# Kernel tuning notes

Measured on AMD Instinct MI355X. Metric: run time of the kernel, lower is better.

Reference implementation:

```python
import jax, jax.numpy as jnp
import numpy as np

B = 32768
STATE_DIM = 64
ACTION_DIM = 16
HIDDEN = 512
ENSEMBLE = 7
TOP_K = 5
IN_DIM = STATE_DIM + ACTION_DIM          # 80
OUT_DIM = 2 * (STATE_DIM + 1)            # 130 (mu | log_std)


def setup_inputs() -> dict:
    key = jax.random.key(0)
    ks = jax.random.split(key, 12)
    state = jax.random.normal(ks[0], (B, STATE_DIM), dtype=jnp.float32)
    action = jax.random.normal(ks[1], (B, ACTION_DIM), dtype=jnp.float32)
    eps = jax.random.normal(ks[2], (B, STATE_DIM + 1), dtype=jnp.float32)
    # per-sample random expert among the selected subset [0, TOP_K)
    idx = jax.random.randint(ks[3], (B,), 0, TOP_K).astype(jnp.int64)
    # stacked expert params (kaiming-ish scale = 1/sqrt(fan_in))
    W1 = jax.random.normal(ks[4], (ENSEMBLE, IN_DIM, HIDDEN), dtype=jnp.float32) / np.sqrt(IN_DIM)
    b1 = jnp.zeros((ENSEMBLE, HIDDEN), dtype=jnp.float32)
    W2 = jax.random.normal(ks[5], (ENSEMBLE, HIDDEN, HIDDEN), dtype=jnp.float32) / np.sqrt(HIDDEN)
    b2 = jnp.zeros((ENSEMBLE, HIDDEN), dtype=jnp.float32)
    W3 = jax.random.normal(ks[6], (ENSEMBLE, HIDDEN, OUT_DIM), dtype=jnp.float32) / np.sqrt(HIDDEN)
    b3 = jnp.zeros((ENSEMBLE, OUT_DIM), dtype=jnp.float32)
    return {"state": state, "action": action, "eps": eps,
            "W1": W1, "b1": b1, "W2": W2, "b2": b2, "W3": W3, "b3": b3,
            "idx": idx}


def reference(state, action, eps, W1, b1, W2, b2, W3, b3, idx):
    # DynamicsEnsemble.predict: per-sample random expert, Gaussian sample.
    x = jnp.concatenate([state, action], axis=-1)            # [B, IN_DIM]
    # run all experts densely, then gather the routed expert per sample
    h = jax.nn.relu(jnp.einsum('bi,eih->beh', x, W1) + b1)   # [B, E, H]
    h = jax.nn.relu(jnp.einsum('beh,ehk->bek', h, W2) + b2)  # [B, E, H]
    o = jnp.einsum('bek,eko->beo', h, W3) + b3               # [B, E, OUT]
    out = jnp.take_along_axis(o, idx[:, None, None].astype(jnp.int32), axis=1)[:, 0]  # [B, OUT]
    d = state.shape[-1] + 1
    mu = out[:, :d]
    log_std = jnp.clip(out[:, d:], -20.0, 2.0)
    y = mu + jnp.exp(log_std) * eps                          # sampled [delta_state, reward]
    next_state = state + y[:, : state.shape[-1]]
    reward = y[:, state.shape[-1]:]                          # [B, 1]
    return next_state, reward
```

## Files before the change

### kernel.cpp

```cpp
#include <hip/hip_runtime.h>
#include <math.h>

#define B_ROWS     32768
#define STATE_DIM  64
#define ACTION_DIM 16
#define HIDDEN     512
#define ENSEMBLE   7
#define TOP_K      5
#define IN_DIM     80
#define OUT_DIM    130
#define D_OUT      65

#define BM         64
#define MTHREADS   1024
#define NTILES     (B_ROWS / BM + TOP_K)

#define L1_K8 12
#define L2_K8 64
#define L3_K8 64
#define L3_N  144

#define N_W1 (TOP_K * L1_K8 * HIDDEN * 8)
#define N_W2 (TOP_K * L2_K8 * HIDDEN * 8)
#define N_W3 (TOP_K * L3_K8 * L3_N * 8)

#define OFF_CNT    0
#define OFF_BUCKET 256
#define OFF_W1     (OFF_BUCKET + ENSEMBLE * B_ROWS * 4)
#define OFF_W2     (OFF_W1 + N_W1 * 2)
#define OFF_W3     (OFF_W2 + N_W2 * 2)
#define WS_NEEDED  ((size_t)(OFF_W3 + N_W3 * 2))

#define BUCKET_BLOCKS ((B_ROWS + 255) / 256)
#define PACK_G        (TOP_K * (L1_K8*HIDDEN + L2_K8*HIDDEN + L3_K8*L3_N))
#define PACK_BLOCKS   ((PACK_G + 255) / 256)

typedef __attribute__((ext_vector_type(8))) _Float16 half8;
typedef __attribute__((ext_vector_type(4))) float f32x4;

__global__ void prep_kernel(const int* __restrict__ idx,
                            int* __restrict__ cnt,
                            int* __restrict__ bucket,
                            const float* __restrict__ W1, const float* __restrict__ W2,
                            const float* __restrict__ W3,
                            _Float16* __restrict__ w1, _Float16* __restrict__ w2,
                            _Float16* __restrict__ w3) {
    if (blockIdx.x < BUCKET_BLOCKS) {
        int b = blockIdx.x * 256 + threadIdx.x;
        int lane = threadIdx.x & 63;
        int e = -1;
        if (b < B_ROWS) e = min(max(idx[b], 0), TOP_K - 1);
        #pragma unroll
        for (int ev = 0; ev < TOP_K; ++ev) {
            unsigned long long m = __ballot(e == ev);
            if (m == 0ull) continue;
            int leader = __ffsll((unsigned long long)m) - 1;
            int base = 0;
            if (lane == leader) base = atomicAdd(&cnt[ev], __popcll(m));
            base = __shfl(base, leader);
            if (e == ev) {
                int rank = __popcll(m & ((1ull << lane) - 1ull));
                bucket[ev * B_ROWS + base + rank] = b;
            }
        }
        return;
    }
    const int G1 = L1_K8 * HIDDEN;
    const int G2 = L2_K8 * HIDDEN;
    const int G3 = L3_K8 * L3_N;
    const int GPE = G1 + G2 + G3;
    int g = (blockIdx.x - BUCKET_BLOCKS) * 256 + threadIdx.x;
    if (g >= TOP_K * GPE) return;
    int e = g / GPE, r = g % GPE;

    const float* src; _Float16* dd;
    size_t dst; int k8, n, Kreal, Nreal, srcN;
    if (r < G1) {
        k8 = r / HIDDEN; n = r % HIDDEN;
        src = W1 + (size_t)e * IN_DIM * HIDDEN; Kreal = IN_DIM; Nreal = HIDDEN; srcN = HIDDEN;
        dd = w1; dst = (((size_t)e * L1_K8 + k8) * HIDDEN + n) * 8;
    } else if (r < G1 + G2) {
        int rr = r - G1; k8 = rr / HIDDEN; n = rr % HIDDEN;
        src = W2 + (size_t)e * HIDDEN * HIDDEN; Kreal = HIDDEN; Nreal = HIDDEN; srcN = HIDDEN;
        dd = w2; dst = (((size_t)e * L2_K8 + k8) * HIDDEN + n) * 8;
    } else {
        int rr = r - G1 - G2; k8 = rr / L3_N; n = rr % L3_N;
        src = W3 + (size_t)e * HIDDEN * OUT_DIM; Kreal = HIDDEN; Nreal = OUT_DIM; srcN = OUT_DIM;
        dd = w3; dst = (((size_t)e * L3_K8 + k8) * L3_N + n) * 8;
    }
    half8 hv;
    #pragma unroll
    for (int j = 0; j < 8; ++j) {
        int k = k8 * 8 + j;
        float v = (k < Kreal && n < Nreal) ? src[(size_t)k * srcN + n] : 0.f;
        hv[j] = (_Float16)v;
    }
    *(half8*)(dd + dst) = hv;
}

template<int ASTR, bool SWZ, int KSTEPS>
__device__ __forceinline__ void gemm_compute(
    const char* A,
    const _Float16* __restrict__ B, int Bn, const float* __restrict__ bias,
    f32x4 (&acc)[2][4], int lane, int row0, int col0)
{
    const int lc = lane & 15, kg = lane >> 4;
    #pragma unroll
    for (int ctl = 0; ctl < 4; ++ctl) {
        float b = bias[col0 + ctl * 16 + lc];
        acc[0][ctl] = (f32x4){b, b, b, b};
        acc[1][ctl] = acc[0][ctl];
    }
    const size_t bstep = (size_t)4 * Bn * 8;
    const _Float16* bp = B + ((size_t)kg * Bn + col0 + lc) * 8;

    #pragma unroll
    for (int ks = 0; ks < KSTEPS; ++ks) {
        half8 bc[4];
        #pragma unroll
        for (int ctl = 0; ctl < 4; ++ctl)
            bc[ctl] = *(const half8*)(bp + (size_t)ks * bstep + ctl * 128);
        half8 ah[2];
        #pragma unroll
        for (int rt = 0; rt < 2; ++rt) {
            int row = row0 + rt * 16 + lc;
            int lin = row * ASTR + ks * 64 + kg * 16;
            if (SWZ) lin ^= (row & 7) << 4;
            ah[rt] = *(const half8*)(A + lin);
        }
        #pragma unroll
        for (int rt = 0; rt < 2; ++rt)
        #pragma unroll
        for (int ctl = 0; ctl < 4; ++ctl)
            acc[rt][ctl] = __builtin_amdgcn_mfma_f32_16x16x32_f16(ah[rt], bc[ctl], acc[rt][ctl], 0, 0, 0);
    }
}

__device__ __forceinline__ void store_h(char* O, f32x4 (&acc)[2][4], int lane, int row0, int col0) {
    const int lc = lane & 15, kg = lane >> 4;
    #pragma unroll
    for (int rt = 0; rt < 2; ++rt)
    #pragma unroll
    for (int ctl = 0; ctl < 4; ++ctl)
    #pragma unroll
    for (int q = 0; q < 4; ++q) {
        int row = row0 + rt * 16 + kg * 4 + q;
        int col = col0 + ctl * 16 + lc;
        float v = fmaxf(acc[rt][ctl][q], 0.f);
        int lin = (row * 1024 + col * 2) ^ ((row & 7) << 4);
        *(_Float16*)(O + lin) = (_Float16)v;
    }
}

__device__ __forceinline__ int xcd_swz(int orig) {
    const int nx = 8, q = NTILES / nx, r = NTILES % nx;
    int xcd = orig % nx, pos = orig / nx;
    int base = (xcd < r) ? xcd * (q + 1) : r * (q + 1) + (xcd - r) * q;
    return base + pos;
}

__launch_bounds__(MTHREADS)
__global__ void mlp_mfma_kernel(const float* __restrict__ state,
                                const float* __restrict__ action,
                                const float* __restrict__ eps,
                                const float* __restrict__ b1,
                                const float* __restrict__ b2,
                                const float* __restrict__ b3,
                                const _Float16* __restrict__ w1,
                                const _Float16* __restrict__ w2,
                                const _Float16* __restrict__ w3,
                                const int* __restrict__ cnt, const int* __restrict__ bucket,
                                float* __restrict__ out) {
    __shared__ char smem[79872];
    char* xs = smem;
    char* hs = smem + 14336;
    float* os = (float*)(smem + 14336);

    const int j = xcd_swz(blockIdx.x);
    int e = TOP_K, base = 0;
    {
        int acct = 0;
        #pragma unroll
        for (int ev = 0; ev < TOP_K; ++ev) {
            int tiles = (cnt[ev] + BM - 1) / BM;
            if (e == TOP_K && j < acct + tiles) { e = ev; base = acct; }
            acct += tiles;
        }
    }
    if (e >= TOP_K) return;
    const int n    = cnt[e];
    const int tile = j - base;
    const int m0   = tile * BM;
    if (m0 >= n) return;
    const int nrows = min(BM, n - m0);
    const int t = threadIdx.x;
    const int lane = t & 63;
    const int wv = t >> 6;
    const int row0 = (wv >> 3) * 32;
    const int col0 = (wv & 7) * 64;
    const int* brow = bucket + (size_t)e * B_ROWS;

    for (int i = t; i < BM * 112; i += MTHREADS) {
        int r = i / 112, c = i % 112;
        int rb = brow[min(m0 + r, n - 1)];
        float v = 0.f;
        if (c < STATE_DIM)      v = state[(size_t)rb * STATE_DIM + c];
        else if (c < IN_DIM)    v = action[(size_t)rb * ACTION_DIM + (c - STATE_DIM)];
        *(_Float16*)(xs + r * 224 + c * 2) = (_Float16)v;
    }
    __syncthreads();

    f32x4 acc[2][4];

    gemm_compute<224, false, 3>(xs,
        w1 + (size_t)e * L1_K8 * HIDDEN * 8,
        HIDDEN, b1 + (size_t)e * HIDDEN, acc, lane, row0, col0);
    store_h(hs, acc, lane, row0, col0);
    __syncthreads();

    gemm_compute<1024, true, 16>(hs,
        w2 + (size_t)e * L2_K8 * HIDDEN * 8,
        HIDDEN, b2 + (size_t)e * HIDDEN, acc, lane, row0, col0);
    __syncthreads();
    store_h(hs, acc, lane, row0, col0);
    __syncthreads();

    {
        const _Float16* Bw = w3 + (size_t)e * L3_K8 * L3_N * 8;
        const float* b3e = b3 + (size_t)e * OUT_DIM;
        const int lc = lane & 15, kg = lane >> 4;
        const int rt  = wv & 3;
        const int ct0 = wv >> 2;
        const bool third = (wv < 4);
        f32x4 o0 = {0.f,0.f,0.f,0.f}, o1 = o0, o2 = o0;
        const size_t bstep = (size_t)4 * L3_N * 8;
        const _Float16* bp0 = Bw + ((size_t)kg * L3_N + ct0 * 16 + lc) * 8;
        const _Float16* bp1 = Bw + ((size_t)kg * L3_N + (ct0 + 4) * 16 + lc) * 8;
        const _Float16* bp2 = Bw + ((size_t)kg * L3_N + 8 * 16 + lc) * 8;

        #pragma unroll
        for (int ks = 0; ks < 16; ++ks) {
            int row = rt * 16 + lc;
            int lin = (row * 1024 + ks * 64 + kg * 16) ^ ((row & 7) << 4);
            half8 ah = *(const half8*)(hs + lin);
            half8 v0 = *(const half8*)(bp0 + (size_t)ks * bstep);
            half8 v1 = *(const half8*)(bp1 + (size_t)ks * bstep);
            o0 = __builtin_amdgcn_mfma_f32_16x16x32_f16(ah, v0, o0, 0, 0, 0);
            o1 = __builtin_amdgcn_mfma_f32_16x16x32_f16(ah, v1, o1, 0, 0, 0);
            if (third) {
                half8 v2 = *(const half8*)(bp2 + (size_t)ks * bstep);
                o2 = __builtin_amdgcn_mfma_f32_16x16x32_f16(ah, v2, o2, 0, 0, 0);
            }
        }
        __syncthreads();
        {
            int c0 = ct0 * 16 + lc;
            int c1 = (ct0 + 4) * 16 + lc;
            #pragma unroll
            for (int q = 0; q < 4; ++q) {
                int row = rt * 16 + kg * 4 + q;
                os[row * 132 + c0] = o0[q] + b3e[c0];
                if (c1 < OUT_DIM) os[row * 132 + c1] = o1[q] + b3e[c1];
            }
            if (third) {
                int c2 = 128 + lc;
                if (c2 < OUT_DIM) {
                    #pragma unroll
                    for (int q = 0; q < 4; ++q) {
                        int row = rt * 16 + kg * 4 + q;
                        os[row * 132 + c2] = o2[q] + b3e[c2];
                    }
                }
            }
        }
    }
    __syncthreads();

    for (int i = t; i < BM * D_OUT; i += MTHREADS) {
        int r = i / D_OUT, c = i % D_OUT;
        if (r >= nrows) continue;
        int rb = brow[m0 + r];
        float mu = os[r * 132 + c];
        float ls = fminf(fmaxf(os[r * 132 + c + D_OUT], -20.f), 2.f);
        float y  = fmaf(expf(ls), eps[(size_t)rb * D_OUT + c], mu);
        if (c < STATE_DIM) {
            out[(size_t)rb * STATE_DIM + c] = state[(size_t)rb * STATE_DIM + c] + y;
        } else {
            out[(size_t)B_ROWS * STATE_DIM + rb] = y;
        }
    }
}

#define FB_BM      16
#define FB_THREADS 256
#define FB_TILES   ((B_ROWS + FB_BM - 1) / FB_BM)

__launch_bounds__(FB_THREADS, 2)
__global__ void mlp_fp32_kernel(const float* __restrict__ state,
                                const float* __restrict__ action,
                                const float* __restrict__ eps,
                                const float* __restrict__ W1, const float* __restrict__ b1,
                                const float* __restrict__ W2, const float* __restrict__ b2,
                                const float* __restrict__ W3, const float* __restrict__ b3,
                                const int* __restrict__ cnt, const int* __restrict__ bucket,
                                float* __restrict__ out) {
    __shared__ float xs[FB_BM][IN_DIM];
    __shared__ float h1[FB_BM][HIDDEN];
    __shared__ float h2[FB_BM][HIDDEN];
    __shared__ float os[FB_BM][OUT_DIM];
    __shared__ int   rows[FB_BM];

    const int e    = blockIdx.x / FB_TILES;
    const int tile = blockIdx.x % FB_TILES;
    const int n    = cnt[e];
    const int m0   = tile * FB_BM;
    if (m0 >= n) return;
    const int nrows = min(FB_BM, n - m0);
    const int t = threadIdx.x;

    if (t < FB_BM) rows[t] = (t < nrows) ? bucket[e * B_ROWS + m0 + t] : bucket[e * B_ROWS + m0];
    __syncthreads();

    for (int i = t; i < FB_BM * IN_DIM; i += FB_THREADS) {
        int r = i / IN_DIM, c = i % IN_DIM;
        int rb = rows[r];
        xs[r][c] = (c < STATE_DIM) ? state[(size_t)rb * STATE_DIM + c]
                                   : action[(size_t)rb * ACTION_DIM + (c - STATE_DIM)];
    }
    __syncthreads();

    const int c0 = 2 * t;
    {
        const float* We = W1 + (size_t)e * IN_DIM * HIDDEN;
        float acc0[FB_BM], acc1[FB_BM];
        const float bias0 = b1[(size_t)e * HIDDEN + c0];
        const float bias1 = b1[(size_t)e * HIDDEN + c0 + 1];
        #pragma unroll
        for (int r = 0; r < FB_BM; ++r) { acc0[r] = bias0; acc1[r] = bias1; }
        for (int k = 0; k < IN_DIM; k += 4) {
            float2 w0 = *(const float2*)&We[(size_t)(k + 0) * HIDDEN + c0];
            float2 w1v = *(const float2*)&We[(size_t)(k + 1) * HIDDEN + c0];
            float2 w2v = *(const float2*)&We[(size_t)(k + 2) * HIDDEN + c0];
            float2 w3v = *(const float2*)&We[(size_t)(k + 3) * HIDDEN + c0];
            #pragma unroll
            for (int r = 0; r < FB_BM; ++r) {
                float4 x = *(const float4*)&xs[r][k];
                acc0[r] = fmaf(x.x, w0.x, acc0[r]); acc1[r] = fmaf(x.x, w0.y, acc1[r]);
                acc0[r] = fmaf(x.y, w1v.x, acc0[r]); acc1[r] = fmaf(x.y, w1v.y, acc1[r]);
                acc0[r] = fmaf(x.z, w2v.x, acc0[r]); acc1[r] = fmaf(x.z, w2v.y, acc1[r]);
                acc0[r] = fmaf(x.w, w3v.x, acc0[r]); acc1[r] = fmaf(x.w, w3v.y, acc1[r]);
            }
        }
        #pragma unroll
        for (int r = 0; r < FB_BM; ++r)
            *(float2*)&h1[r][c0] = make_float2(fmaxf(acc0[r], 0.f), fmaxf(acc1[r], 0.f));
    }
    __syncthreads();
    {
        const float* We = W2 + (size_t)e * HIDDEN * HIDDEN;
        float acc0[FB_BM], acc1[FB_BM];
        const float bias0 = b2[(size_t)e * HIDDEN + c0];
        const float bias1 = b2[(size_t)e * HIDDEN + c0 + 1];
        #pragma unroll
        for (int r = 0; r < FB_BM; ++r) { acc0[r] = bias0; acc1[r] = bias1; }
        for (int k = 0; k < HIDDEN; k += 4) {
            float2 w0 = *(const float2*)&We[(size_t)(k + 0) * HIDDEN + c0];
            float2 w1v = *(const float2*)&We[(size_t)(k + 1) * HIDDEN + c0];
            float2 w2v = *(const float2*)&We[(size_t)(k + 2) * HIDDEN + c0];
            float2 w3v = *(const float2*)&We[(size_t)(k + 3) * HIDDEN + c0];
            #pragma unroll
            for (int r = 0; r < FB_BM; ++r) {
                float4 x = *(const float4*)&h1[r][k];
                acc0[r] = fmaf(x.x, w0.x, acc0[r]); acc1[r] = fmaf(x.x, w0.y, acc1[r]);
                acc0[r] = fmaf(x.y, w1v.x, acc0[r]); acc1[r] = fmaf(x.y, w1v.y, acc1[r]);
                acc0[r] = fmaf(x.z, w2v.x, acc0[r]); acc1[r] = fmaf(x.z, w2v.y, acc1[r]);
                acc0[r] = fmaf(x.w, w3v.x, acc0[r]); acc1[r] = fmaf(x.w, w3v.y, acc1[r]);
            }
        }
        #pragma unroll
        for (int r = 0; r < FB_BM; ++r)
            *(float2*)&h2[r][c0] = make_float2(fmaxf(acc0[r], 0.f), fmaxf(acc1[r], 0.f));
    }
    __syncthreads();
    {
        const float* We = W3 + (size_t)e * HIDDEN * OUT_DIM;
        for (int i = t; i < FB_BM * OUT_DIM; i += FB_THREADS) {
            int r = i / OUT_DIM, c = i % OUT_DIM;
            float acc = b3[(size_t)e * OUT_DIM + c];
            for (int k = 0; k < HIDDEN; k += 4) {
                float4 h = *(const float4*)&h2[r][k];
                acc = fmaf(h.x, We[(size_t)(k + 0) * OUT_DIM + c], acc);
                acc = fmaf(h.y, We[(size_t)(k + 1) * OUT_DIM + c], acc);
                acc = fmaf(h.z, We[(size_t)(k + 2) * OUT_DIM + c], acc);
                acc = fmaf(h.w, We[(size_t)(k + 3) * OUT_DIM + c], acc);
            }
            os[r][c] = acc;
        }
    }
    __syncthreads();
    for (int i = t; i < FB_BM * D_OUT; i += FB_THREADS) {
        int r = i / D_OUT, c = i % D_OUT;
        if (r >= nrows) continue;
        int rb = rows[r];
        float mu = os[r][c];
        float ls = fminf(fmaxf(os[r][c + D_OUT], -20.f), 2.f);
        float y  = fmaf(expf(ls), eps[(size_t)rb * D_OUT + c], mu);
        if (c < STATE_DIM) out[(size_t)rb * STATE_DIM + c] = state[(size_t)rb * STATE_DIM + c] + y;
        else               out[(size_t)B_ROWS * STATE_DIM + rb] = y;
    }
}

extern "C" void kernel_launch(void* const* d_in, const int* in_sizes, int n_in,
                              void* d_out, int out_size, void* d_ws, size_t ws_size,
                              hipStream_t stream) {
    const float* state  = (const float*)d_in[0];
    const float* action = (const float*)d_in[1];
    const float* eps    = (const float*)d_in[2];
    const float* W1     = (const float*)d_in[3];
    const float* b1     = (const float*)d_in[4];
    const float* W2     = (const float*)d_in[5];
    const float* b2     = (const float*)d_in[6];
    const float* W3     = (const float*)d_in[7];
    const float* b3     = (const float*)d_in[8];
    const int*   idx    = (const int*)d_in[9];
    float* out = (float*)d_out;

    int* cnt    = (int*)((char*)d_ws + OFF_CNT);
    int* bucket = (int*)((char*)d_ws + OFF_BUCKET);

    hipMemsetAsync(cnt, 0, ENSEMBLE * sizeof(int), stream);

    if (ws_size >= WS_NEEDED) {
        _Float16* w1 = (_Float16*)((char*)d_ws + OFF_W1);
        _Float16* w2 = (_Float16*)((char*)d_ws + OFF_W2);
        _Float16* w3 = (_Float16*)((char*)d_ws + OFF_W3);

        prep_kernel<<<BUCKET_BLOCKS + PACK_BLOCKS, 256, 0, stream>>>(
            idx, cnt, bucket, W1, W2, W3, w1, w2, w3);

        mlp_mfma_kernel<<<NTILES, MTHREADS, 0, stream>>>(
            state, action, eps, b1, b2, b3, w1, w2, w3, cnt, bucket, out);
    } else {
        prep_kernel<<<BUCKET_BLOCKS, 256, 0, stream>>>(
            idx, cnt, bucket, W1, W2, W3, (_Float16*)0, (_Float16*)0, (_Float16*)0);
        mlp_fp32_kernel<<<TOP_K * FB_TILES, FB_THREADS, 0, stream>>>(
            state, action, eps, W1, b1, W2, b2, W3, b3, cnt, bucket, out);
    }
}
```

Measured before the change: 136.9 us.

## Halve block threads and give each wave a full 64-row by 64-column tile

Drops the block from 1024 to 512 threads (8 waves). Each wave now computes all 64 rows for its 64-column slice, using a 4x4 grid of MFMA accumulators instead of 2x4. This halves how often B weights are fetched per row and reuses each B fragment across four row tiles. The layer-3 split is rebalanced so each wave handles four or five column tiles. In exchange, per-thread register use roughly doubles, which can limit occupancy even with launch bounds asking for 4 blocks per CU, and there are fewer waves to hide latency.

Result: slower. 155.2 us (+13.3%).

```diff
diff --git a/kernel.cpp b/kernel.cpp
--- a/kernel.cpp
+++ b/kernel.cpp
@@ -12,7 +12,7 @@
 #define D_OUT      65
 
 #define BM         64
-#define MTHREADS   1024
+#define MTHREADS   512
 #define NTILES     (B_ROWS / BM + TOP_K)
 
 #define L1_K8 12
@@ -102,14 +102,14 @@
 __device__ __forceinline__ void gemm_compute(
     const char* A,
     const _Float16* __restrict__ B, int Bn, const float* __restrict__ bias,
-    f32x4 (&acc)[2][4], int lane, int row0, int col0)
+    f32x4 (&acc)[4][4], int lane, int col0)
 {
     const int lc = lane & 15, kg = lane >> 4;
     #pragma unroll
     for (int ctl = 0; ctl < 4; ++ctl) {
         float b = bias[col0 + ctl * 16 + lc];
-        acc[0][ctl] = (f32x4){b, b, b, b};
-        acc[1][ctl] = acc[0][ctl];
+        #pragma unroll
+        for (int rt = 0; rt < 4; ++rt) acc[rt][ctl] = (f32x4){b, b, b, b};
     }
     const size_t bstep = (size_t)4 * Bn * 8;
     const _Float16* bp = B + ((size_t)kg * Bn + col0 + lc) * 8;
@@ -120,31 +120,31 @@
         #pragma unroll
         for (int ctl = 0; ctl < 4; ++ctl)
             bc[ctl] = *(const half8*)(bp + (size_t)ks * bstep + ctl * 128);
-        half8 ah[2];
-        #pragma unroll
-        for (int rt = 0; rt < 2; ++rt) {
-            int row = row0 + rt * 16 + lc;
+        half8 ah[4];
+        #pragma unroll
+        for (int rt = 0; rt < 4; ++rt) {
+            int row = rt * 16 + lc;
             int lin = row * ASTR + ks * 64 + kg * 16;
             if (SWZ) lin ^= (row & 7) << 4;
             ah[rt] = *(const half8*)(A + lin);
         }
         #pragma unroll
-        for (int rt = 0; rt < 2; ++rt)
+        for (int rt = 0; rt < 4; ++rt)
         #pragma unroll
         for (int ctl = 0; ctl < 4; ++ctl)
             acc[rt][ctl] = __builtin_amdgcn_mfma_f32_16x16x32_f16(ah[rt], bc[ctl], acc[rt][ctl], 0, 0, 0);
     }
 }
 
-__device__ __forceinline__ void store_h(char* O, f32x4 (&acc)[2][4], int lane, int row0, int col0) {
+__device__ __forceinline__ void store_h(char* O, f32x4 (&acc)[4][4], int lane, int col0) {
     const int lc = lane & 15, kg = lane >> 4;
     #pragma unroll
-    for (int rt = 0; rt < 2; ++rt)
+    for (int rt = 0; rt < 4; ++rt)
     #pragma unroll
     for (int ctl = 0; ctl < 4; ++ctl)
     #pragma unroll
     for (int q = 0; q < 4; ++q) {
-        int row = row0 + rt * 16 + kg * 4 + q;
+        int row = rt * 16 + kg * 4 + q;
         int col = col0 + ctl * 16 + lc;
         float v = fmaxf(acc[rt][ctl][q], 0.f);
         int lin = (row * 1024 + col * 2) ^ ((row & 7) << 4);
@@ -159,7 +159,7 @@
     return base + pos;
 }
 
-__launch_bounds__(MTHREADS)
+__launch_bounds__(MTHREADS, 4)
 __global__ void mlp_mfma_kernel(const float* __restrict__ state,
                                 const float* __restrict__ action,
                                 const float* __restrict__ eps,
@@ -196,8 +196,7 @@
     const int t = threadIdx.x;
     const int lane = t & 63;
     const int wv = t >> 6;
-    const int row0 = (wv >> 3) * 32;
-    const int col0 = (wv & 7) * 64;
+    const int col0 = wv * 64;
     const int* brow = bucket + (size_t)e * B_ROWS;
 
     for (int i = t; i < BM * 112; i += MTHREADS) {
@@ -210,19 +209,19 @@
     }
     __syncthreads();
 
-    f32x4 acc[2][4];
+    f32x4 acc[4][4];
 
     gemm_compute<224, false, 3>(xs,
         w1 + (size_t)e * L1_K8 * HIDDEN * 8,
-        HIDDEN, b1 + (size_t)e * HIDDEN, acc, lane, row0, col0);
-    store_h(hs, acc, lane, row0, col0);
+        HIDDEN, b1 + (size_t)e * HIDDEN, acc, lane, col0);
+    store_h(hs, acc, lane, col0);
     __syncthreads();
 
     gemm_compute<1024, true, 16>(hs,
         w2 + (size_t)e * L2_K8 * HIDDEN * 8,
-        HIDDEN, b2 + (size_t)e * HIDDEN, acc, lane, row0, col0);
-    __syncthreads();
-    store_h(hs, acc, lane, row0, col0);
+        HIDDEN, b2 + (size_t)e * HIDDEN, acc, lane, col0);
+    __syncthreads();
+    store_h(hs, acc, lane, col0);
     __syncthreads();
 
     {
@@ -231,12 +230,14 @@
         const int lc = lane & 15, kg = lane >> 4;
         const int rt  = wv & 3;
         const int ct0 = wv >> 2;
-        const bool third = (wv < 4);
-        f32x4 o0 = {0.f,0.f,0.f,0.f}, o1 = o0, o2 = o0;
+        const bool fifth = (wv < 4);
+        f32x4 o0 = {0.f,0.f,0.f,0.f}, o1 = o0, o2 = o0, o3 = o0, o4 = o0;
         const size_t bstep = (size_t)4 * L3_N * 8;
-        const _Float16* bp0 = Bw + ((size_t)kg * L3_N + ct0 * 16 + lc) * 8;
-        const _Float16* bp1 = Bw + ((size_t)kg * L3_N + (ct0 + 4) * 16 + lc) * 8;
-        const _Float16* bp2 = Bw + ((size_t)kg * L3_N + 8 * 16 + lc) * 8;
+        const _Float16* bp0 = Bw + ((size_t)kg * L3_N + (ct0 + 0) * 16 + lc) * 8;
+        const _Float16* bp1 = Bw + ((size_t)kg * L3_N + (ct0 + 2) * 16 + lc) * 8;
+        const _Float16* bp2 = Bw + ((size_t)kg * L3_N + (ct0 + 4) * 16 + lc) * 8;
+        const _Float16* bp3 = Bw + ((size_t)kg * L3_N + (ct0 + 6) * 16 + lc) * 8;
+        const _Float16* bp4 = Bw + ((size_t)kg * L3_N + 8 * 16 + lc) * 8;
 
         #pragma unroll
         for (int ks = 0; ks < 16; ++ks) {
@@ -245,30 +246,38 @@
             half8 ah = *(const half8*)(hs + lin);
             half8 v0 = *(const half8*)(bp0 + (size_t)ks * bstep);
             half8 v1 = *(const half8*)(bp1 + (size_t)ks * bstep);
+            half8 v2 = *(const half8*)(bp2 + (size_t)ks * bstep);
+            half8 v3 = *(const half8*)(bp3 + (size_t)ks * bstep);
             o0 = __builtin_amdgcn_mfma_f32_16x16x32_f16(ah, v0, o0, 0, 0, 0);
             o1 = __builtin_amdgcn_mfma_f32_16x16x32_f16(ah, v1, o1, 0, 0, 0);
-            if (third) {
-                half8 v2 = *(const half8*)(bp2 + (size_t)ks * bstep);
-                o2 = __builtin_amdgcn_mfma_f32_16x16x32_f16(ah, v2, o2, 0, 0, 0);
+            o2 = __builtin_amdgcn_mfma_f32_16x16x32_f16(ah, v2, o2, 0, 0, 0);
+            o3 = __builtin_amdgcn_mfma_f32_16x16x32_f16(ah, v3, o3, 0, 0, 0);
+            if (fifth) {
+                half8 v4 = *(const half8*)(bp4 + (size_t)ks * bstep);
+                o4 = __builtin_amdgcn_mfma_f32_16x16x32_f16(ah, v4, o4, 0, 0, 0);
             }
         }
         __syncthreads();
         {
-            int c0 = ct0 * 16 + lc;
-            int c1 = (ct0 + 4) * 16 + lc;
+            int c0 = (ct0 + 0) * 16 + lc;
+            int c1 = (ct0 + 2) * 16 + lc;
+            int c2 = (ct0 + 4) * 16 + lc;
+            int c3 = (ct0 + 6) * 16 + lc;
             #pragma unroll
             for (int q = 0; q < 4; ++q) {
                 int row = rt * 16 + kg * 4 + q;
                 os[row * 132 + c0] = o0[q] + b3e[c0];
-                if (c1 < OUT_DIM) os[row * 132 + c1] = o1[q] + b3e[c1];
-            }
-            if (third) {
-                int c2 = 128 + lc;
-                if (c2 < OUT_DIM) {
+                os[row * 132 + c1] = o1[q] + b3e[c1];
+                os[row * 132 + c2] = o2[q] + b3e[c2];
+                os[row * 132 + c3] = o3[q] + b3e[c3];
+            }
+            if (fifth) {
+                int c4 = 128 + lc;
+                if (c4 < OUT_DIM) {
                     #pragma unroll
                     for (int q = 0; q < 4; ++q) {
                         int row = rt * 16 + kg * 4 + q;
-                        os[row * 132 + c2] = o2[q] + b3e[c2];
+                        os[row * 132 + c4] = o4[q] + b3e[c4];
                     }
                 }
             }
```

## Stage weight tiles into LDS with async global_load_lds double buffering

Applied to the files above, without the earlier changes.

Raises the row tile to 112 rows with 512 threads and one block per CU. Weights are repacked in prep into contiguous 16KB k-slices, which are streamed into two LDS buffers with global_load_lds while MFMAs run on the previous slice. Each wave now computes 7 row-tiles by 4 column-tiles, so every B fragment is reused across more rows and direct global weight reads from each wave are removed. The cost is much more LDS (144KB), a __syncthreads per k-slice, higher register pressure from 28 accumulators, and fewer waves per CU.

Measured after the change: 210.0 us. 1.53x slower.

```diff
diff --git a/kernel.cpp b/kernel.cpp
--- a/kernel.cpp
+++ b/kernel.cpp
@@ -11,8 +11,8 @@
 #define OUT_DIM    130
 #define D_OUT      65
 
-#define BM         64
-#define MTHREADS   1024
+#define BM         112
+#define MTHREADS   512
 #define NTILES     (B_ROWS / BM + TOP_K)
 
 #define L1_K8 12
@@ -37,6 +37,14 @@
 
 typedef __attribute__((ext_vector_type(8))) _Float16 half8;
 typedef __attribute__((ext_vector_type(4))) float f32x4;
+
+__device__ __forceinline__ void stage_tile(const char* g, char* l, int t, int bytes) {
+    for (int off = t * 16; off < bytes; off += MTHREADS * 16) {
+        __builtin_amdgcn_global_load_lds(
+            (const __attribute__((address_space(1))) void*)(g + off),
+            (__attribute__((address_space(3))) void*)(l + off), 16, 0, 0);
+    }
+}
 
 __global__ void prep_kernel(const int* __restrict__ idx,
                             int* __restrict__ cnt,
@@ -78,11 +86,15 @@
     if (r < G1) {
         k8 = r / HIDDEN; n = r % HIDDEN;
         src = W1 + (size_t)e * IN_DIM * HIDDEN; Kreal = IN_DIM; Nreal = HIDDEN; srcN = HIDDEN;
-        dd = w1; dst = (((size_t)e * L1_K8 + k8) * HIDDEN + n) * 8;
+        dd = w1;
+        int kt = k8 >> 2, kgp = k8 & 3, hf = n >> 8, c = n & 255;
+        dst = ((size_t)(((e * 3 + kt) * 2 + hf) * 4 + kgp)) * 2048 + (size_t)c * 8;
     } else if (r < G1 + G2) {
         int rr = r - G1; k8 = rr / HIDDEN; n = rr % HIDDEN;
         src = W2 + (size_t)e * HIDDEN * HIDDEN; Kreal = HIDDEN; Nreal = HIDDEN; srcN = HIDDEN;
-        dd = w2; dst = (((size_t)e * L2_K8 + k8) * HIDDEN + n) * 8;
+        dd = w2;
+        int kt = k8 >> 2, kgp = k8 & 3, hf = n >> 8, c = n & 255;
+        dst = ((size_t)(((e * 16 + kt) * 2 + hf) * 4 + kgp)) * 2048 + (size_t)c * 8;
     } else {
         int rr = r - G1 - G2; k8 = rr / L3_N; n = rr % L3_N;
         src = W3 + (size_t)e * HIDDEN * OUT_DIM; Kreal = HIDDEN; Nreal = OUT_DIM; srcN = OUT_DIM;
@@ -98,57 +110,59 @@
     *(half8*)(dd + dst) = hv;
 }
 
-template<int ASTR, bool SWZ, int KSTEPS>
-__device__ __forceinline__ void gemm_compute(
-    const char* A,
-    const _Float16* __restrict__ B, int Bn, const float* __restrict__ bias,
-    f32x4 (&acc)[2][4], int lane, int row0, int col0)
+template<int ASTR, bool SWZ, int NU>
+__device__ __forceinline__ void gemm_staged(
+    const char* A, const char* Bsrc, const float* __restrict__ bias,
+    char* b0, char* b1, f32x4 (&acc)[7][4], int t, int lane, int wv)
 {
     const int lc = lane & 15, kg = lane >> 4;
     #pragma unroll
-    for (int ctl = 0; ctl < 4; ++ctl) {
-        float b = bias[col0 + ctl * 16 + lc];
-        acc[0][ctl] = (f32x4){b, b, b, b};
-        acc[1][ctl] = acc[0][ctl];
-    }
-    const size_t bstep = (size_t)4 * Bn * 8;
-    const _Float16* bp = B + ((size_t)kg * Bn + col0 + lc) * 8;
-
+    for (int g = 0; g < 4; ++g) {
+        float b = bias[(g >> 1) * 256 + wv * 32 + (g & 1) * 16 + lc];
+        #pragma unroll
+        for (int rt = 0; rt < 7; ++rt) acc[rt][g] = (f32x4){b, b, b, b};
+    }
+    half8 ah[7];
     #pragma unroll
-    for (int ks = 0; ks < KSTEPS; ++ks) {
-        half8 bc[4];
-        #pragma unroll
-        for (int ctl = 0; ctl < 4; ++ctl)
-            bc[ctl] = *(const half8*)(bp + (size_t)ks * bstep + ctl * 128);
-        half8 ah[2];
-        #pragma unroll
-        for (int rt = 0; rt < 2; ++rt) {
-            int row = row0 + rt * 16 + lc;
-            int lin = row * ASTR + ks * 64 + kg * 16;
-            if (SWZ) lin ^= (row & 7) << 4;
-            ah[rt] = *(const half8*)(A + lin);
-        }
-        #pragma unroll
-        for (int rt = 0; rt < 2; ++rt)
-        #pragma unroll
-        for (int ctl = 0; ctl < 4; ++ctl)
-            acc[rt][ctl] = __builtin_amdgcn_mfma_f32_16x16x32_f16(ah[rt], bc[ctl], acc[rt][ctl], 0, 0, 0);
-    }
-}
-
-__device__ __forceinline__ void store_h(char* O, f32x4 (&acc)[2][4], int lane, int row0, int col0) {
+    for (int u = 0; u < NU; ++u) {
+        if (u + 1 < NU)
+            stage_tile(Bsrc + (size_t)(u + 1) * 16384, ((u + 1) & 1) ? b1 : b0, t, 16384);
+        const char* bb = (u & 1) ? b1 : b0;
+        const int ks = u >> 1;
+        if ((u & 1) == 0) {
+            #pragma unroll
+            for (int rt = 0; rt < 7; ++rt) {
+                int row = rt * 16 + lc;
+                int lin = row * ASTR + ks * 64 + kg * 16;
+                if (SWZ) lin ^= (row & 7) << 4;
+                ah[rt] = *(const half8*)(A + lin);
+            }
+        }
+        half8 bc0 = *(const half8*)(bb + (kg * 256 + wv * 32 + lc) * 16);
+        half8 bc1 = *(const half8*)(bb + (kg * 256 + wv * 32 + 16 + lc) * 16);
+        const int g0 = (u & 1) * 2;
+        #pragma unroll
+        for (int rt = 0; rt < 7; ++rt) {
+            acc[rt][g0 + 0] = __builtin_amdgcn_mfma_f32_16x16x32_f16(ah[rt], bc0, acc[rt][g0 + 0], 0, 0, 0);
+            acc[rt][g0 + 1] = __builtin_amdgcn_mfma_f32_16x16x32_f16(ah[rt], bc1, acc[rt][g0 + 1], 0, 0, 0);
+        }
+        __syncthreads();
+    }
+}
+
+__device__ __forceinline__ void store_h(char* O, f32x4 (&acc)[7][4], int lane, int wv) {
     const int lc = lane & 15, kg = lane >> 4;
     #pragma unroll
-    for (int rt = 0; rt < 2; ++rt)
+    for (int rt = 0; rt < 7; ++rt)
     #pragma unroll
-    for (int ctl = 0; ctl < 4; ++ctl)
-    #pragma unroll
-    for (int q = 0; q < 4; ++q) {
-        int row = row0 + rt * 16 + kg * 4 + q;
-        int col = col0 + ctl * 16 + lc;
-        float v = fmaxf(acc[rt][ctl][q], 0.f);
-        int lin = (row * 1024 + col * 2) ^ ((row & 7) << 4);
-        *(_Float16*)(O + lin) = (_Float16)v;
+    for (int g = 0; g < 4; ++g) {
+        int col = (g >> 1) * 256 + wv * 32 + (g & 1) * 16 + lc;
+        #pragma unroll
+        for (int q = 0; q < 4; ++q) {
+            int row = rt * 16 + kg * 4 + q;
+            int lin = (row * 1024 + col * 2) ^ ((row & 7) << 4);
+            *(_Float16*)(O + lin) = (_Float16)fmaxf(acc[rt][g][q], 0.f);
+        }
     }
 }
 
@@ -159,7 +173,7 @@
     return base + pos;
 }
 
-__launch_bounds__(MTHREADS)
+__launch_bounds__(MTHREADS, 1)
 __global__ void mlp_mfma_kernel(const float* __restrict__ state,
                                 const float* __restrict__ action,
                                 const float* __restrict__ eps,
@@ -171,10 +185,12 @@
                                 const _Float16* __restrict__ w3,
                                 const int* __restrict__ cnt, const int* __restrict__ bucket,
                                 float* __restrict__ out) {
-    __shared__ char smem[79872];
+    __shared__ char smem[147456];
+    char* hs = smem;
     char* xs = smem;
-    char* hs = smem + 14336;
-    float* os = (float*)(smem + 14336);
+    float* os = (float*)smem;
+    char* bb0 = smem + 114688;
+    char* bb1 = smem + 131072;
 
     const int j = xcd_swz(blockIdx.x);
     int e = TOP_K, base = 0;
@@ -196,10 +212,14 @@
     const int t = threadIdx.x;
     const int lane = t & 63;
     const int wv = t >> 6;
-    const int row0 = (wv >> 3) * 32;
-    const int col0 = (wv & 7) * 64;
+    const int lc = lane & 15, kg = lane >> 4;
     const int* brow = bucket + (size_t)e * B_ROWS;
 
+    const char* w1b = (const char*)w1 + (size_t)e * 6  * 16384;
+    const char* w2b = (const char*)w2 + (size_t)e * 32 * 16384;
+    const char* w3b = (const char*)w3 + (size_t)e * 16 * 9216;
+
+    stage_tile(w1b, bb0, t, 16384);
     for (int i = t; i < BM * 112; i += MTHREADS) {
         int r = i / 112, c = i % 112;
         int rb = brow[min(m0 + r, n - 1)];
@@ -210,66 +230,52 @@
     }
     __syncthreads();
 
-    f32x4 acc[2][4];
-
-    gemm_compute<224, false, 3>(xs,
-        w1 + (size_t)e * L1_K8 * HIDDEN * 8,
-        HIDDEN, b1 + (size_t)e * HIDDEN, acc, lane, row0, col0);
-    store_h(hs, acc, lane, row0, col0);
-    __syncthreads();
-
-    gemm_compute<1024, true, 16>(hs,
-        w2 + (size_t)e * L2_K8 * HIDDEN * 8,
-        HIDDEN, b2 + (size_t)e * HIDDEN, acc, lane, row0, col0);
-    __syncthreads();
-    store_h(hs, acc, lane, row0, col0);
+    f32x4 acc[7][4];
+
+    gemm_staged<224, false, 6>(xs, w1b, b1 + (size_t)e * HIDDEN, bb0, bb1, acc, t, lane, wv);
+    store_h(hs, acc, lane, wv);
+    stage_tile(w2b, bb0, t, 16384);
+    __syncthreads();
+
+    gemm_staged<1024, true, 32>(hs, w2b, b2 + (size_t)e * HIDDEN, bb0, bb1, acc, t, lane, wv);
+    store_h(hs, acc, lane, wv);
+    stage_tile(w3b, bb0, t, 9216);
     __syncthreads();
 
     {
-        const _Float16* Bw = w3 + (size_t)e * L3_K8 * L3_N * 8;
         const float* b3e = b3 + (size_t)e * OUT_DIM;
-        const int lc = lane & 15, kg = lane >> 4;
-        const int rt  = wv & 3;
-        const int ct0 = wv >> 2;
-        const bool third = (wv < 4);
-        f32x4 o0 = {0.f,0.f,0.f,0.f}, o1 = o0, o2 = o0;
-        const size_t bstep = (size_t)4 * L3_N * 8;
-        const _Float16* bp0 = Bw + ((size_t)kg * L3_N + ct0 * 16 + lc) * 8;
-        const _Float16* bp1 = Bw + ((size_t)kg * L3_N + (ct0 + 4) * 16 + lc) * 8;
-        const _Float16* bp2 = Bw + ((size_t)kg * L3_N + 8 * 16 + lc) * 8;
-
-        #pragma unroll
-        for (int ks = 0; ks < 16; ++ks) {
-            int row = rt * 16 + lc;
-            int lin = (row * 1024 + ks * 64 + kg * 16) ^ ((row & 7) << 4);
-            half8 ah = *(const half8*)(hs + lin);
-            half8 v0 = *(const half8*)(bp0 + (size_t)ks * bstep);
-            half8 v1 = *(const half8*)(bp1 + (size_t)ks * bstep);
-            o0 = __builtin_amdgcn_mfma_f32_16x16x32_f16(ah, v0, o0, 0, 0, 0);
-            o1 = __builtin_amdgcn_mfma_f32_16x16x32_f16(ah, v1, o1, 0, 0, 0);
-            if (third) {
-                half8 v2 = *(const half8*)(bp2 + (size_t)ks * bstep);
-                o2 = __builtin_amdgcn_mfma_f32_16x16x32_f16(ah, v2, o2, 0, 0, 0);
-            }
-        }
-        __syncthreads();
-        {
-            int c0 = ct0 * 16 + lc;
-            int c1 = (ct0 + 4) * 16 + lc;
+        f32x4 o[8];
+        #pragma unroll
+        for (int jj = 0; jj < 8; ++jj) o[jj] = (f32x4){0.f, 0.f, 0.f, 0.f};
+        #pragma unroll
+        for (int u = 0; u < 16; ++u) {
+            if (u + 1 < 16)
+                stage_tile(w3b + (size_t)(u + 1) * 9216, ((u + 1) & 1) ? bb1 : bb0, t, 9216);
+            const char* bb = (u & 1) ? bb1 : bb0;
             #pragma unroll
-            for (int q = 0; q < 4; ++q) {
-                int row = rt * 16 + kg * 4 + q;
-                os[row * 132 + c0] = o0[q] + b3e[c0];
-                if (c1 < OUT_DIM) os[row * 132 + c1] = o1[q] + b3e[c1];
-            }
-            if (third) {
-                int c2 = 128 + lc;
-                if (c2 < OUT_DIM) {
+            for (int jj = 0; jj < 8; ++jj) {
+                int U = wv * 8 + jj;
+                if (U < 63) {
+                    int rt = U / 9, ct = U % 9;
+                    int row = rt * 16 + lc;
+                    int lin = (row * 1024 + u * 64 + kg * 16) ^ ((row & 7) << 4);
+                    half8 ah = *(const half8*)(hs + lin);
+                    half8 bh = *(const half8*)(bb + (kg * 144 + ct * 16 + lc) * 16);
+                    o[jj] = __builtin_amdgcn_mfma_f32_16x16x32_f16(ah, bh, o[jj], 0, 0, 0);
+                }
+            }
+            __syncthreads();
+        }
+        #pragma unroll
+        for (int jj = 0; jj < 8; ++jj) {
+            int U = wv * 8 + jj;
+            if (U < 63) {
+                int rt = U / 9, ct = U % 9;
+                int col = ct * 16 + lc;
+                if (col < OUT_DIM) {
                     #pragma unroll
-                    for (int q = 0; q < 4; ++q) {
-                        int row = rt * 16 + kg * 4 + q;
-                        os[row * 132 + c2] = o2[q] + b3e[c2];
-                    }
+                    for (int q = 0; q < 4; ++q)
+                        os[(rt * 16 + kg * 4 + q) * 132 + col] = o[jj][q] + b3e[col];
                 }
             }
         }
```
